# Performance work log

Measured on AMD Instinct MI355X. Metric: run time of the kernel, lower is better.

Reference implementation:

```python
import jax, jax.numpy as jnp
import numpy as np

B, C, H, W = 8, 3, 512, 512
KH = KW = 17          # blur kernel
F_REG, D = 24, 4      # regularization filters, Wiener filters
RKH = RKW = 5         # reg-filter kernel size


def psf2otf(psf, shape):
    """Zero-pad psf to `shape`, circshift so center is at (0,0), FFT."""
    kh, kw = psf.shape[-2:]
    Ho, Wo = shape
    pad = [(0, 0)] * (psf.ndim - 2) + [(0, Ho - kh), (0, Wo - kw)]
    p = jnp.pad(psf, pad)
    p = jnp.roll(p, (-(kh // 2), -(kw // 2)), axis=(-2, -1))
    return jnp.fft.fft2(p)


def edgetaper(img, psf):
    """MATLAB-style edgetaper. img: (C,Hp,Wp), psf: (kh,kw)."""
    Ho, Wo = img.shape[-2:]

    def autocorr(proj, n):
        z = jnp.zeros((n,), img.dtype).at[: proj.shape[0]].set(proj)
        z = jnp.fft.ifft(jnp.abs(jnp.fft.fft(z)) ** 2).real
        z = jnp.concatenate([z, z[:1]])  # length n+1
        return z / z.max()

    beta0 = autocorr(psf.sum(1), Ho - 1)  # (Ho,)
    beta1 = autocorr(psf.sum(0), Wo - 1)  # (Wo,)
    alpha = (1.0 - beta0)[:, None] * (1.0 - beta1)[None, :]  # (Ho,Wo)
    blurred = jnp.fft.ifft2(jnp.fft.fft2(img) * psf2otf(psf, (Ho, Wo))).real
    return alpha * img + (1.0 - alpha) * blurred


def wiener_one(y, psf, g, log_alpha):
    """Multi-filter Wiener deconvolution for one image.
    y: (C,Hp,Wp), psf: (kh,kw), g: (F,1,rkh,rkw), log_alpha: (D,1).
    Returns (D,C,Hp,Wp)."""
    Ho, Wo = y.shape[-2:]
    K = psf2otf(psf, (Ho, Wo))                  # (Hp,Wp) complex
    G = psf2otf(g[:, 0], (Ho, Wo))              # (F,Hp,Wp)
    Greg = jnp.sum(jnp.abs(G) ** 2, axis=0)     # (Hp,Wp)
    Y = jnp.fft.fft2(y)                         # (C,Hp,Wp)
    a = jnp.exp(log_alpha)[:, :, None, None]    # (D,1,1,1)
    S = jnp.abs(K) ** 2 + a * Greg              # (D,1,Hp,Wp)
    X = (jnp.conj(K) * Y)[None] / S             # (D,C,Hp,Wp)
    return jnp.fft.ifft2(X).real


def forward(image, blurKernel, stdn, wiener_conv_weights, wiener_scale, alpha, weights):
    kh, kw = blurKernel.shape[-2:]
    # getPad2RetainShape
    pt, pb = (kh + 1) // 2 - 1, kh - (kh + 1) // 2
    pl, pr = (kw + 1) // 2 - 1, kw - (kw + 1) // 2
    x = jnp.pad(image, ((0, 0), (0, 0), (pt, pb), (pl, pr)), mode='symmetric')
    psf = blurKernel[:, 0]                      # (B,kh,kw)
    x = jax.vmap(edgetaper)(x, psf)             # (B,C,Hp,Wp)
    # WeightNormalization: zero-mean then L2-normalize per filter, times scale
    w = wiener_conv_weights - wiener_conv_weights.mean(axis=(1, 2, 3), keepdims=True)
    nrm = jnp.sqrt(jnp.sum(w * w, axis=(1, 2, 3), keepdims=True))
    w = w * (wiener_scale.reshape(-1, 1, 1, 1) / nrm)
    xw = jax.vmap(lambda yi, ki: wiener_one(yi, ki, w, alpha))(x, psf)  # (B,D,C,Hp,Wp)
    Hp, Wp = x.shape[-2:]
    crop = xw[..., pt:Hp - pb, pl:Wp - pr]      # Crop2D back to (H,W)
    return jnp.sum(crop * weights, axis=1)      # weighted mix over D -> (B,C,H,W)


def setup_inputs() -> dict:
    key = jax.random.key(0)
    ks = jax.random.split(key, 4)
    image = jax.random.uniform(ks[0], (B, C, H, W), jnp.float32)
    k = jax.random.uniform(ks[1], (B, 1, KH, KW), jnp.float32)
    blurKernel = k / jnp.sum(k, axis=(-2, -1), keepdims=True)  # normalized psf
    stdn = jax.random.uniform(ks[2], (B,), jnp.float32) * 0.05 + 0.01
    wiener_conv_weights = jax.random.normal(ks[3], (F_REG, 1, RKH, RKW), jnp.float32)
    wiener_scale = jnp.full((F_REG,), 0.1, jnp.float32)
    alpha = jnp.log(jnp.logspace(np.log10(1e-3), np.log10(1e-1), D))[:, None].astype(jnp.float32)
    weights = jnp.full((1, D, 1, 1, 1), 1.0 / D, jnp.float32)
    return {"image": image, "blurKernel": blurKernel, "stdn": stdn,
            "wiener_conv_weights": wiener_conv_weights, "wiener_scale": wiener_scale,
            "alpha": alpha, "weights": weights}


def reference(image, blurKernel, stdn, wiener_conv_weights, wiener_scale, alpha, weights):
    return forward(image, blurKernel, stdn, wiener_conv_weights, wiener_scale, alpha, weights)
```

## Files before the change

### kernel.cpp

```cpp
#include <hip/hip_runtime.h>
#include <hip/hip_bf16.h>

#define NN 528
#define NP (NN*NN)
#define IMG 512
#define IMGP (IMG*IMG)
#define PAD 8
#define KH 17
#define KT (KH*KH)
#define NF 24
#define RK 5
#define RKT (RK*RK)
#define ND 4
#define TOPB (17*NN)
#define ROWB (2*TOPB)
#define SIDEB (494*34)
#define BORD (ROWB + SIDEB)

static __device__ __forceinline__ float ldx(const void* p, long i, int bf) {
    if (bf) return __bfloat162float(((const __hip_bfloat16*)p)[i]);
    return ((const float*)p)[i];
}

static __device__ __forceinline__ int gmap(int m) {
    if (m < -8)  return 495 - m;
    if (m < 0)   return -m - 1;
    if (m < 512) return m;
    if (m < 520) return 1023 - m;
    return 527 - m;
}

__global__ void detect_k(const void* pimg, int nimg, const void* pbk, int nbk,
                         const void* pwcw, int nwcw, const void* pws, int nws,
                         const float* c4a, const float* c4b,
                         int* __restrict__ flags,
                         float* __restrict__ alpha_ws, float* __restrict__ wgt_ws) {
    int t = threadIdx.x;
    const void* ps[4] = {pimg, pbk, pwcw, pws};
    int ns[4] = {nimg, nbk, nwcw, nws};
    if (t < 4) {
        const unsigned short* q = (const unsigned short*)ps[t];
        int n = ns[t];
        int K = n < 512 ? n : 512;
        int cnt = 0, pass = 0;
        for (int i = 0; i < K; i += 2) {
            int e = (q[i] >> 7) & 0xFF;
            pass += (e >= 100 && e <= 140);
            cnt++;
        }
        flags[t] = (pass * 10 >= cnt * 8) ? 1 : 0;
    }
    if (t == 7) {
        const float* A = (c4a[0] < 0.f) ? c4a : c4b;
        const float* W = (c4a[0] < 0.f) ? c4b : c4a;
        for (int i = 0; i < ND; ++i) { alpha_ws[i] = A[i]; wgt_ws[i] = W[i]; }
    }
}

__global__ void twinit_k(float2* __restrict__ twN) {
    int i = blockIdx.x * blockDim.x + threadIdx.x;
    if (i < NN) {
        double th = -6.283185307179586476925287 * (double)i / (double)NN;
        twN[i] = make_float2((float)cos(th), (float)sin(th));
    }
}

__global__ void wnorm_k(const void* __restrict__ wcw, const void* __restrict__ wscale,
                        const int* __restrict__ flags, float* __restrict__ wout) {
    int f = threadIdx.x;
    if (f >= NF) return;
    int bfw = flags[2], bfs = flags[3];
    float v[RKT];
    float mean = 0.f;
    for (int i = 0; i < RKT; ++i) { v[i] = ldx(wcw, f*RKT+i, bfw); mean += v[i]; }
    mean *= (1.f/(float)RKT);
    float ss = 0.f;
    for (int i = 0; i < RKT; ++i) { v[i] -= mean; ss += v[i]*v[i]; }
    float sc = ldx(wscale, f, bfs) / sqrtf(ss);
    for (int i = 0; i < RKT; ++i) wout[f*RKT+i] = v[i]*sc;
}

__global__ void prep_k(const void* __restrict__ blurKernel, const int* __restrict__ flags,
                       float* __restrict__ psf_all, float* __restrict__ A0_all,
                       float* __restrict__ A1_all) {
    int b = blockIdx.x, t = threadIdx.x;
    int bf = flags[1];
    __shared__ float psf[KT];
    __shared__ float q0[KH], q1[KH], ac0[KH], ac1[KH];
    for (int i = t; i < KT; i += 64) {
        float v = ldx(blurKernel, b*KT + i, bf);
        psf[i] = v;
        psf_all[b*KT + i] = v;
    }
    __syncthreads();
    if (t < KH) {
        float s0 = 0.f, s1 = 0.f;
        for (int k = 0; k < KH; ++k) { s0 += psf[t*KH + k]; s1 += psf[k*KH + t]; }
        q0[t] = s0; q1[t] = s1;
    }
    __syncthreads();
    if (t < KH) {
        float a0 = 0.f, a1 = 0.f;
        for (int m = 0; m + t < KH; ++m) { a0 += q0[m]*q0[m+t]; a1 += q1[m]*q1[m+t]; }
        ac0[t] = a0; ac1[t] = a1;
    }
    __syncthreads();
    for (int r = t; r < NN; r += 64) {
        int lag = min(r, (NN-1) - r);
        float b0 = (lag <= KH-1) ? ac0[lag]/ac0[0] : 0.f;
        float b1 = (lag <= KH-1) ? ac1[lag]/ac1[0] : 0.f;
        A0_all[b*NN + r] = 1.f - b0;
        A1_all[b*NN + r] = 1.f - b1;
    }
}

__global__ void greg_k(const float* __restrict__ w, const float2* __restrict__ twN,
                       float* __restrict__ Greg) {
    int p = blockIdx.x * blockDim.x + threadIdx.x;
    if (p >= NP) return;
    int u = p % NN, v = p / NN;
    float2 rp[RK], cp[RK];
    for (int j = 0; j < RK; ++j) {
        int m = (u * (j - RK/2)) % NN; if (m < 0) m += NN;
        rp[j] = twN[m];
    }
    for (int k = 0; k < RK; ++k) {
        int m = (v * (k - RK/2)) % NN; if (m < 0) m += NN;
        cp[k] = twN[m];
    }
    float pr[RKT], pi[RKT];
    for (int j = 0; j < RK; ++j)
        for (int k = 0; k < RK; ++k) {
            pr[j*RK+k] = rp[j].x*cp[k].x - rp[j].y*cp[k].y;
            pi[j*RK+k] = rp[j].x*cp[k].y + rp[j].y*cp[k].x;
        }
    float acc = 0.f;
    for (int f = 0; f < NF; ++f) {
        float gr = 0.f, gi = 0.f;
        for (int i = 0; i < RKT; ++i) {
            float wv = w[f*RKT + i];
            gr += wv * pr[i];
            gi += wv * pi[i];
        }
        acc += gr*gr + gi*gi;
    }
    Greg[p] = acc;
}

__global__ __launch_bounds__(256)
void border2_k(const void* __restrict__ image, const int* __restrict__ flags,
               const float* __restrict__ psf_all,
               const float* __restrict__ A0_all, const float* __restrict__ A1_all,
               float* __restrict__ borderV) {
    __shared__ float4 S4[1440];
    float* S = (float*)S4;
    int bp = blockIdx.y;
    int b = bp / 3;
    long ofs = (long)bp * IMGP;
    int bf = flags[0];
    int t = threadIdx.x;
    const float* pw = psf_all + b*KT;
    int bx = blockIdx.x;

    if (bx < 20) {
        int q = bx >> 1, h = bx & 1;
        int r0;
        if (q < 4) r0 = 4*q;
        else if (q == 4) r0 = 13;
        else if (q < 9) r0 = 511 + 4*(q-5);
        else r0 = 524;
        int X0 = h * 264;
        for (int idx = t; idx < 20*288; idx += 256) {
            int i = idx / 288, xi = idx - i*288;
            int x = X0 + xi;
            float v = 0.f;
            if (x < 544) {
                int sr = gmap(r0 - 16 + i);
                int sc = gmap(x - 16);
                v = ldx(image, ofs + (long)sr*IMG + sc, bf);
            }
            S[idx] = v;
        }
        __syncthreads();
        for (int g = t; g < 264; g += 256) {
            int rx = g / 66, cl = g - rx*66;
            int c0 = X0 + 4*cl;
            int x0 = 4*cl;
            float acc0 = 0.f, acc1 = 0.f, acc2 = 0.f, acc3 = 0.f;
            for (int j = 0; j < KH; ++j) {
                const float4* SjV = (const float4*)(S + (16 + rx - j)*288 + x0);
                float xv[20];
                #pragma unroll
                for (int qv = 0; qv < 5; ++qv) {
                    float4 tv = SjV[qv];
                    xv[4*qv+0] = tv.x; xv[4*qv+1] = tv.y;
                    xv[4*qv+2] = tv.z; xv[4*qv+3] = tv.w;
                }
                const float* wj = pw + j*KH;
                #pragma unroll
                for (int qq = 0; qq < 20; ++qq) {
                    {int k = 0 + 16 - qq; if (k >= 0 && k < KH) acc0 += wj[k]*xv[qq];}
                    {int k = 1 + 16 - qq; if (k >= 0 && k < KH) acc1 += wj[k]*xv[qq];}
                    {int k = 2 + 16 - qq; if (k >= 0 && k < KH) acc2 += wj[k]*xv[qq];}
                    {int k = 3 + 16 - qq; if (k >= 0 && k < KH) acc3 += wj[k]*xv[qq];}
                }
            }
            int r = r0 + rx;
            float a0v = A0_all[b*NN + r];
            int ibase = (r < 17) ? r*NN : TOPB + (r-511)*NN;
            float accs[4] = {acc0, acc1, acc2, acc3};
            #pragma unroll
            for (int d = 0; d < 4; ++d) {
                int c = c0 + d;
                float xo = S[(8 + rx)*288 + (x0 + 8 + d)];
                float al = a0v * A1_all[b*NN + c];
                borderV[(size_t)bp*BORD + ibase + c] = al*xo + (1.f - al)*accs[d];
            }
        }
    } else {
        int chunk = bx - 20;
        int r0 = 17 + 26*chunk;
        for (int idx = t; idx < 42*84; idx += 256) {
            int i = idx / 84, x = idx - i*84;
            float v = 0.f;
            int m = -1000;
            if (x < 33) m = x - 16;
            else if (x >= 48 && x < 81) m = x - 48 + 495;
            if (m != -1000) {
                int sr = gmap(r0 - 16 + i);
                int sc = gmap(m);
                v = ldx(image, ofs + (long)sr*IMG + sc, bf);
            }
            S[idx] = v;
        }
        __syncthreads();
        int g = t;
        if (g < 208) {
            int ry = g >> 3, s = g & 7;
            int c0 = (s < 4) ? 4*s : 511 + 4*(s-4);
            int sz = ((s & 3) == 3) ? 5 : 4;
            int x0 = (s < 4) ? 4*s : 48 + 4*(s-4);
            float acc0=0.f, acc1=0.f, acc2=0.f, acc3=0.f, acc4=0.f;
            for (int j = 0; j < KH; ++j) {
                const float4* SjV = (const float4*)(S + (16 + ry - j)*84 + x0);
                float xv[24];
                #pragma unroll
                for (int qv = 0; qv < 6; ++qv) {
                    float4 tv = SjV[qv];
                    xv[4*qv+0] = tv.x; xv[4*qv+1] = tv.y;
                    xv[4*qv+2] = tv.z; xv[4*qv+3] = tv.w;
                }
                const float* wj = pw + j*KH;
                #pragma unroll
                for (int qq = 0; qq < 21; ++qq) {
                    {int k = 0 + 16 - qq; if (k >= 0 && k < KH) acc0 += wj[k]*xv[qq];}
                    {int k = 1 + 16 - qq; if (k >= 0 && k < KH) acc1 += wj[k]*xv[qq];}
                    {int k = 2 + 16 - qq; if (k >= 0 && k < KH) acc2 += wj[k]*xv[qq];}
                    {int k = 3 + 16 - qq; if (k >= 0 && k < KH) acc3 += wj[k]*xv[qq];}
                    {int k = 4 + 16 - qq; if (k >= 0 && k < KH) acc4 += wj[k]*xv[qq];}
                }
            }
            int r = r0 + ry;
            float a0v = A0_all[b*NN + r];
            int cc0 = (s < 4) ? c0 : c0 - 494;
            size_t ib = (size_t)bp*BORD + ROWB + (size_t)(r-17)*34 + cc0;
            float accs[5] = {acc0, acc1, acc2, acc3, acc4};
            #pragma unroll
            for (int d = 0; d < 5; ++d) {
                if (d < sz) {
                    int c = c0 + d;
                    float xo = S[(8 + ry)*84 + (x0 + 8 + d)];
                    float al = a0v * A1_all[b*NN + c];
                    borderV[ib + d] = al*xo + (1.f - al)*accs[d];
                }
            }
        }
    }
}

__global__ void kv_k(const float* __restrict__ psf_all, const float2* __restrict__ twN,
                     float2* __restrict__ Sv) {
    int idx = blockIdx.x * blockDim.x + threadIdx.x;
    if (idx >= 8*NN*KH) return;
    int j = idx % KH;
    int rest = idx / KH;
    int v = rest % NN, b = rest / NN;
    int m = (520 * v) % NN;
    float sr = 0.f, si = 0.f;
    const float* ps = psf_all + b*KT + j*KH;
    for (int k = 0; k < KH; ++k) {
        float2 cp = twN[m];
        m += v; if (m >= NN) m -= NN;
        sr += ps[k] * cp.x;
        si += ps[k] * cp.y;
    }
    Sv[idx] = make_float2(sr, si);
}

__global__ __launch_bounds__(128)
void fftrow_k(const void* __restrict__ image, const int* __restrict__ flags,
              const float* __restrict__ borderV, const float2* __restrict__ twN,
              float2* __restrict__ buf, int B0) {
    __shared__ float2 X[NN];
    __shared__ float2 A[NN];
    __shared__ float2 TW[NN];
    int t = threadIdx.x;
    int q = blockIdx.x / NN;
    int r = blockIdx.x - q*NN;
    int pair = q / 3, ch = q - 3*pair;
    int b0p = B0 + 2*pair;
    int bf = flags[0];
    for (int i = t; i < NN; i += 128) TW[i] = twN[i];
    for (int c = t; c < NN; c += 128) {
        float x0, x1;
        bool isb = (r < 17) | (r >= 511) | (c < 17) | (c >= 511);
        if (isb) {
            int i2;
            if (r < 17) i2 = r*NN + c;
            else if (r >= 511) i2 = TOPB + (r-511)*NN + c;
            else { int cc = (c < 17) ? c : c - 494; i2 = ROWB + (r-17)*34 + cc; }
            x0 = borderV[(size_t)(b0p*3 + ch)*BORD + i2];
            x1 = borderV[(size_t)((b0p+1)*3 + ch)*BORD + i2];
        } else {
            long ofs0 = ((long)b0p*3 + ch) * IMGP + (long)(r - PAD)*IMG + (c - PAD);
            x0 = ldx(image, ofs0, bf);
            x1 = ldx(image, ofs0 + 3L*IMGP, bf);
        }
        X[c] = make_float2(x0, x1);
    }
    __syncthreads();
    for (int o = t; o < NN; o += 128) {
        int n1 = o & 15, k2 = o >> 4;
        float ar = 0.f, ai = 0.f;
        int m = 0;
        for (int n2 = 0; n2 < 33; ++n2) {
            float2 xv = X[n1 + 16*n2];
            float2 w = TW[m * 16];
            ar += xv.x*w.x - xv.y*w.y;
            ai += xv.x*w.y + xv.y*w.x;
            m += k2; if (m >= 33) m -= 33;
        }
        float2 tw = TW[n1 * k2];
        A[n1*33 + k2] = make_float2(ar*tw.x - ai*tw.y, ar*tw.y + ai*tw.x);
    }
    __syncthreads();
    float2* dst = buf + (size_t)q*NP + (size_t)r*NN;
    for (int o = t; o < NN; o += 128) {
        int k1 = o / 33, k2 = o - 33*k1;
        float ar = 0.f, ai = 0.f;
        int m = 0;
        for (int n1 = 0; n1 < 16; ++n1) {
            float2 bv = A[n1*33 + k2];
            float2 w = TW[m * 33];
            ar += bv.x*w.x - bv.y*w.y;
            ai += bv.x*w.y + bv.y*w.x;
            m = (m + k1) & 15;
        }
        dst[o] = make_float2(ar, ai);
    }
}

__global__ void transpose_ip_k(float2* __restrict__ buf) {
    int tnum = blockIdx.x;
    int ti = 0, rem = tnum;
    while (rem >= 33 - ti) { rem -= 33 - ti; ti++; }
    int tj = ti + rem;
    float2* pl = buf + (size_t)blockIdx.z * NP;
    __shared__ float2 ta[16][17], tb[16][17];
    int tx = threadIdx.x, ty = threadIdx.y;
    int ra = ti*16 + ty, ca = tj*16 + tx;
    int rb = tj*16 + ty, cb = ti*16 + tx;
    ta[ty][tx] = pl[(size_t)ra*NN + ca];
    tb[ty][tx] = pl[(size_t)rb*NN + cb];
    __syncthreads();
    pl[(size_t)ra*NN + ca] = tb[tx][ty];
    pl[(size_t)rb*NN + cb] = ta[tx][ty];
}

__global__ __launch_bounds__(256)
void rowpipe_k(float2* __restrict__ buf, const float2* __restrict__ Sv,
               const float* __restrict__ Greg, const float2* __restrict__ twN,
               const float* __restrict__ alpha4, const float* __restrict__ wgt4, int B0) {
    __shared__ float2 X[2][NN];
    __shared__ float2 A[2][NN];
    __shared__ float2 TW[NN];
    __shared__ float2 SvL[2][KH];
    int t = threadIdx.x;
    int q = blockIdx.x;
    int plane = blockIdx.y;
    int pair = plane / 3;
    int b0p = B0 + 2*pair;
    int qm = (NN - q) % NN;
    int nrow = (qm == q) ? 1 : 2;
    float2* pl = buf + (size_t)plane * NP;
    for (int i = t; i < NN; i += 256) TW[i] = twN[i];
    if (t < 2*KH) {
        int bsel = t / KH, j = t - KH*bsel;
        SvL[bsel][j] = Sv[((size_t)(b0p + bsel)*NN + q)*KH + j];
    }
    for (int i = t; i < nrow*NN; i += 256) {
        int l = i / NN, o = i - l*NN;
        X[l][o] = pl[(size_t)(l ? qm : q)*NN + o];
    }
    __syncthreads();
    for (int i = t; i < nrow*NN; i += 256) {
        int l = i / NN, o = i - l*NN;
        int n1 = o & 15, k2 = o >> 4;
        float ar = 0.f, ai = 0.f;
        int m = 0;
        for (int n2 = 0; n2 < 33; ++n2) {
            float2 xv = X[l][n1 + 16*n2];
            float2 w = TW[m * 16];
            ar += xv.x*w.x - xv.y*w.y;
            ai += xv.x*w.y + xv.y*w.x;
            m += k2; if (m >= 33) m -= 33;
        }
        float2 tw = TW[n1 * k2];
        A[l][n1*33 + k2] = make_float2(ar*tw.x - ai*tw.y, ar*tw.y + ai*tw.x);
    }
    __syncthreads();
    for (int i = t; i < nrow*NN; i += 256) {
        int l = i / NN, o = i - l*NN;
        int k1 = o / 33, k2 = o - 33*k1;
        float ar = 0.f, ai = 0.f;
        int m = 0;
        for (int n1 = 0; n1 < 16; ++n1) {
            float2 bv = A[l][n1*33 + k2];
            float2 w = TW[m * 33];
            ar += bv.x*w.x - bv.y*w.y;
            ai += bv.x*w.y + bv.y*w.x;
            m = (m + k1) & 15;
        }
        X[l][o] = make_float2(ar, ai);
    }
    __syncthreads();
    float aE[ND], wE[ND];
    #pragma unroll
    for (int d = 0; d < ND; ++d) { aE[d] = __expf(alpha4[d]); wE[d] = wgt4[d]; }
    int npair = (nrow == 2) ? NN : 265;
    int lm = nrow - 1;
    for (int k = t; k < npair; k += 256) {
        int km = (NN - k) % NN;
        int mu = (520 * k) % NN;
        float K0r = 0.f, K0i = 0.f, K1r = 0.f, K1i = 0.f;
        for (int j = 0; j < KH; ++j) {
            float2 rp = TW[mu]; mu += k; if (mu >= NN) mu -= NN;
            float2 s0 = SvL[0][j], s1 = SvL[1][j];
            K0r += rp.x*s0.x - rp.y*s0.y;  K0i += rp.x*s0.y + rp.y*s0.x;
            K1r += rp.x*s1.x - rp.y*s1.y;  K1i += rp.x*s1.y + rp.y*s1.x;
        }
        float gg = Greg[(size_t)q*NN + k];
        float K20 = K0r*K0r + K0i*K0i;
        float K21 = K1r*K1r + K1i*K1i;
        float s0a = 0.f, s1a = 0.f;
        #pragma unroll
        for (int d = 0; d < ND; ++d) {
            s0a += wE[d] / fmaxf(K20 + aE[d]*gg, 1e-30f);
            s1a += wE[d] / fmaxf(K21 + aE[d]*gg, 1e-30f);
        }
        s0a *= (1.f/(float)NP);
        s1a *= (1.f/(float)NP);
        float W0r = K0r*s0a, W0i = -K0i*s0a;
        float W1r = K1r*s1a, W1i = -K1i*s1a;
        float2 Z  = X[0][k];
        float2 Zm = X[lm][km];
        float X0r = 0.5f*(Z.x + Zm.x), X0i = 0.5f*(Z.y - Zm.y);
        float X1r = 0.5f*(Z.y + Zm.y), X1i = 0.5f*(Zm.x - Z.x);
        float Y0r = X0r*W0r - X0i*W0i, Y0i = X0r*W0i + X0i*W0r;
        float Y1r = X1r*W1r - X1i*W1i, Y1i = X1r*W1i + X1i*W1r;
        X[0][k]   = make_float2(Y0r - Y1i, Y0i + Y1r);
        X[lm][km] = make_float2(Y0r + Y1i, Y1r - Y0i);
    }
    __syncthreads();
    for (int i = t; i < nrow*NN; i += 256) {
        int l = i / NN, o = i - l*NN;
        int n1 = o & 15, k2 = o >> 4;
        float ar = 0.f, ai = 0.f;
        int m = 0;
        for (int n2 = 0; n2 < 33; ++n2) {
            float2 xv = X[l][n1 + 16*n2];
            float2 w = TW[m * 16];
            float wr = w.x, wi = -w.y;
            ar += xv.x*wr - xv.y*wi;
            ai += xv.x*wi + xv.y*wr;
            m += k2; if (m >= 33) m -= 33;
        }
        float2 tw = TW[n1 * k2];
        float twr = tw.x, twi = -tw.y;
        A[l][n1*33 + k2] = make_float2(ar*twr - ai*twi, ar*twi + ai*twr);
    }
    __syncthreads();
    for (int i = t; i < nrow*NN; i += 256) {
        int l = i / NN, o = i - l*NN;
        int k1 = o / 33, k2 = o - 33*k1;
        float ar = 0.f, ai = 0.f;
        int m = 0;
        for (int n1 = 0; n1 < 16; ++n1) {
            float2 bv = A[l][n1*33 + k2];
            float2 w = TW[m * 33];
            float wr = w.x, wi = -w.y;
            ar += bv.x*wr - bv.y*wi;
            ai += bv.x*wi + bv.y*wr;
            m = (m + k1) & 15;
        }
        X[l][o] = make_float2(ar, ai);
    }
    __syncthreads();
    for (int i = t; i < nrow*NN; i += 256) {
        int l = i / NN, o = i - l*NN;
        pl[(size_t)(l ? qm : q)*NN + o] = X[l][o];
    }
}

__global__ __launch_bounds__(128)
void fft_crop_k(const float2* __restrict__ in, float* __restrict__ out,
                const float2* __restrict__ twN, int B0) {
    __shared__ float2 X[NN];
    __shared__ float2 A[NN];
    __shared__ float2 TW[NN];
    int t = threadIdx.x;
    int q = blockIdx.x >> 9;
    int rp = (blockIdx.x & 511) + PAD;
    int pair = q / 3, ch = q - 3*pair;
    int b0p = B0 + 2*pair;
    const float2* src = in + (size_t)q*NP + (size_t)rp*NN;
    for (int i = t; i < NN; i += 128) { X[i] = src[i]; TW[i] = twN[i]; }
    __syncthreads();
    const float s = -1.f;
    for (int o = t; o < NN; o += 128) {
        int n1 = o & 15, k2 = o >> 4;
        float ar = 0.f, ai = 0.f;
        int m = 0;
        for (int n2 = 0; n2 < 33; ++n2) {
            float2 xv = X[n1 + 16*n2];
            float2 w = TW[m * 16];
            float wr = w.x, wi = w.y * s;
            ar += xv.x*wr - xv.y*wi;
            ai += xv.x*wi + xv.y*wr;
            m += k2; if (m >= 33) m -= 33;
        }
        float2 tw = TW[n1 * k2];
        float twr = tw.x, twi = tw.y * s;
        A[n1*33 + k2] = make_float2(ar*twr - ai*twi, ar*twi + ai*twr);
    }
    __syncthreads();
    float* o0 = out + ((size_t)b0p*3 + ch) * IMGP + (size_t)(rp - PAD) * IMG;
    float* o1 = o0 + 3L*IMGP;
    for (int o = PAD + t; o < IMG + PAD; o += 128) {
        int k1 = o / 33, k2 = o - 33*k1;
        float ar = 0.f, ai = 0.f;
        int m = 0;
        for (int n1 = 0; n1 < 16; ++n1) {
            float2 bv = A[n1*33 + k2];
            float2 w = TW[m * 33];
            float wr = w.x, wi = w.y * s;
            ar += bv.x*wr - bv.y*wi;
            ai += bv.x*wi + bv.y*wr;
            m = (m + k1) & 15;
        }
        o0[o - PAD] = ar;
        o1[o - PAD] = ai;
    }
}

extern "C" void kernel_launch(void* const* d_in, const int* in_sizes, int n_in,
                              void* d_out, int out_size, void* d_ws, size_t ws_size,
                              hipStream_t stream) {
    int i_img = -1, i_bk = -1, i_wcw = -1, i_ws = -1, i_4a = -1, i_4b = -1;
    for (int i = 0; i < n_in; ++i) {
        int s = in_sizes[i];
        if (s == 8*3*IMG*IMG)   i_img = i;
        else if (s == 8*KT)     i_bk = i;
        else if (s == NF*RKT)   i_wcw = i;
        else if (s == NF)       i_ws = i;
        else if (s == ND) { if (i_4a < 0) i_4a = i; else i_4b = i; }
    }
    if (i_img < 0) i_img = 0;
    if (i_bk  < 0) i_bk  = 1;
    if (i_wcw < 0) i_wcw = 3;
    if (i_ws  < 0) i_ws  = 4;
    if (i_4a  < 0) i_4a  = 5;
    if (i_4b  < 0) i_4b  = i_4a;
    const void* image      = d_in[i_img];
    const void* blurKernel = d_in[i_bk];
    const void* wcw        = d_in[i_wcw];
    const void* wscale     = d_in[i_ws];
    const float* c4a       = (const float*)d_in[i_4a];
    const float* c4b       = (const float*)d_in[i_4b];
    float* out = (float*)d_out;

    char* base = (char*)d_ws;
    int*    flags    = (int*)(base);
    float*  alpha_ws = (float*)(base + 64);
    float*  wgt_ws   = (float*)(base + 80);
    float2* twN      = (float2*)(base + 256);
    float*  wnorm    = (float*)(base + 4480);
    float*  psf_all  = (float*)(base + 6880);
    float*  A0       = (float*)(base + 16128);
    float*  A1       = (float*)(base + 33024);
    float*  Greg     = (float*)(base + 49920);
    float2* buf      = (float2*)(base + 1165056);
    float*  borderV  = (float*)(base + 14546688);
    float2* Sv       = (float2*)(base + 17882496);

    if (ws_size < 18456960) return;

    detect_k<<<1, 64, 0, stream>>>(image, in_sizes[i_img], blurKernel, in_sizes[i_bk],
                                   wcw, in_sizes[i_wcw], wscale, in_sizes[i_ws],
                                   c4a, c4b, flags, alpha_ws, wgt_ws);
    twinit_k<<<(NN+63)/64, 64, 0, stream>>>(twN);
    wnorm_k<<<1, 64, 0, stream>>>(wcw, wscale, flags, wnorm);
    prep_k<<<8, 64, 0, stream>>>(blurKernel, flags, psf_all, A0, A1);
    greg_k<<<(NP+255)/256, 256, 0, stream>>>(wnorm, twN, Greg);
    kv_k<<<(8*NN*KH+255)/256, 256, 0, stream>>>(psf_all, twN, Sv);

    dim3 bgrid2(39, 24);
    border2_k<<<bgrid2, 256, 0, stream>>>(image, flags, psf_all, A0, A1, borderV);

    dim3 tblk(16, 16);
    dim3 tgrid6(561, 1, 6);
    dim3 rpgrid(265, 6);
    for (int B0 = 0; B0 < 8; B0 += 4) {
        fftrow_k<<<6*NN, 128, 0, stream>>>(image, flags, borderV, twN, buf, B0);
        transpose_ip_k<<<tgrid6, tblk, 0, stream>>>(buf);
        rowpipe_k<<<rpgrid, 256, 0, stream>>>(buf, Sv, Greg, twN, alpha_ws, wgt_ws, B0);
        transpose_ip_k<<<tgrid6, tblk, 0, stream>>>(buf);
        fft_crop_k<<<6*IMG, 128, 0, stream>>>(buf, out, twN, B0);
    }
}
```

Baseline: 491.3 us.

## Register-block 528-point DFT stages four outputs per thread with vectorized LDS reads

Restructures both stages of the 16x33 mixed-radix DFT used in the row, Wiener and crop kernels so each thread computes four outputs. Each twiddle load is shared across those outputs and operands come from float4 shared-memory reads. Compact 33- and 16-entry twiddle tables and a padded A stride of 34 are added for aligned vector access. The aim is fewer LDS instructions and less index arithmetic per output. The cost is fewer active threads per stage (132 or 144 groups instead of 528 items), so the 128- and 256-thread blocks are underused in places.

```diff
diff --git a/kernel.cpp b/kernel.cpp
--- a/kernel.cpp
+++ b/kernel.cpp
@@ -16,6 +16,7 @@
 #define ROWB (2*TOPB)
 #define SIDEB (494*34)
 #define BORD (ROWB + SIDEB)
+#define AST 34
 
 static __device__ __forceinline__ float ldx(const void* p, long i, int bf) {
     if (bf) return __bfloat162float(((const __hip_bfloat16*)p)[i]);
@@ -28,6 +29,60 @@
     if (m < 512) return m;
     if (m < 520) return 1023 - m;
     return 527 - m;
+}
+
+static __device__ __forceinline__ void s1_group(const float2* __restrict__ Xrow,
+                                                float2* __restrict__ Arow,
+                                                const float2* __restrict__ TWF,
+                                                const float2* __restrict__ T33,
+                                                float s, int grp) {
+    int k2 = grp >> 2, n1b = (grp & 3) << 2;
+    const float4* Xv = (const float4*)Xrow;
+    float ar[4] = {0.f,0.f,0.f,0.f}, ai[4] = {0.f,0.f,0.f,0.f};
+    int m = 0;
+    for (int n2 = 0; n2 < 33; ++n2) {
+        int fi = (n1b + 16*n2) >> 1;
+        float4 a0 = Xv[fi], a1 = Xv[fi+1];
+        float2 w = T33[m]; m += k2; if (m >= 33) m -= 33;
+        float wr = w.x, wi = s*w.y;
+        ar[0] += a0.x*wr - a0.y*wi; ai[0] += a0.x*wi + a0.y*wr;
+        ar[1] += a0.z*wr - a0.w*wi; ai[1] += a0.z*wi + a0.w*wr;
+        ar[2] += a1.x*wr - a1.y*wi; ai[2] += a1.x*wi + a1.y*wr;
+        ar[3] += a1.z*wr - a1.w*wi; ai[3] += a1.z*wi + a1.w*wr;
+    }
+    #pragma unroll
+    for (int j = 0; j < 4; ++j) {
+        float2 tw = TWF[(n1b + j) * k2];
+        float twr = tw.x, twi = s*tw.y;
+        Arow[(n1b + j)*AST + k2] = make_float2(ar[j]*twr - ai[j]*twi, ar[j]*twi + ai[j]*twr);
+    }
+}
+
+static __device__ __forceinline__ void s2_compute(const float2* __restrict__ Arow,
+                                                  const float2* __restrict__ T16,
+                                                  float s, int k1, int k2b, int sz,
+                                                  float* __restrict__ ar, float* __restrict__ ai) {
+    ar[0]=ar[1]=ar[2]=ar[3]=0.f; ai[0]=ai[1]=ai[2]=ai[3]=0.f;
+    if (sz == 4) {
+        const float4* Av = (const float4*)Arow;
+        for (int n1 = 0; n1 < 16; ++n1) {
+            int fi = (n1*AST + k2b) >> 1;
+            float4 a0 = Av[fi], a1 = Av[fi+1];
+            float2 w = T16[(k1*n1) & 15];
+            float wr = w.x, wi = s*w.y;
+            ar[0] += a0.x*wr - a0.y*wi; ai[0] += a0.x*wi + a0.y*wr;
+            ar[1] += a0.z*wr - a0.w*wi; ai[1] += a0.z*wi + a0.w*wr;
+            ar[2] += a1.x*wr - a1.y*wi; ai[2] += a1.x*wi + a1.y*wr;
+            ar[3] += a1.z*wr - a1.w*wi; ai[3] += a1.z*wi + a1.w*wr;
+        }
+    } else {
+        for (int n1 = 0; n1 < 16; ++n1) {
+            float2 a = Arow[n1*AST + k2b];
+            float2 w = T16[(k1*n1) & 15];
+            float wr = w.x, wi = s*w.y;
+            ar[0] += a.x*wr - a.y*wi; ai[0] += a.x*wi + a.y*wr;
+        }
+    }
 }
 
 __global__ void detect_k(const void* pimg, int nimg, const void* pbk, int nbk,
@@ -301,16 +356,20 @@
 void fftrow_k(const void* __restrict__ image, const int* __restrict__ flags,
               const float* __restrict__ borderV, const float2* __restrict__ twN,
               float2* __restrict__ buf, int B0) {
-    __shared__ float2 X[NN];
-    __shared__ float2 A[NN];
-    __shared__ float2 TW[NN];
+    __shared__ __align__(16) float2 X[NN];
+    __shared__ __align__(16) float2 A[16*AST];
+    __shared__ float2 TWF[NN];
+    __shared__ float2 T33[33];
+    __shared__ float2 T16[16];
     int t = threadIdx.x;
     int q = blockIdx.x / NN;
     int r = blockIdx.x - q*NN;
     int pair = q / 3, ch = q - 3*pair;
     int b0p = B0 + 2*pair;
     int bf = flags[0];
-    for (int i = t; i < NN; i += 128) TW[i] = twN[i];
+    for (int i = t; i < NN; i += 128) TWF[i] = twN[i];
+    if (t < 33) T33[t] = twN[t*16];
+    else if (t >= 64 && t < 80) T16[t-64] = twN[(t-64)*33];
     for (int c = t; c < NN; c += 128) {
         float x0, x1;
         bool isb = (r < 17) | (r >= 511) | (c < 17) | (c >= 511);
@@ -329,34 +388,17 @@
         X[c] = make_float2(x0, x1);
     }
     __syncthreads();
-    for (int o = t; o < NN; o += 128) {
-        int n1 = o & 15, k2 = o >> 4;
-        float ar = 0.f, ai = 0.f;
-        int m = 0;
-        for (int n2 = 0; n2 < 33; ++n2) {
-            float2 xv = X[n1 + 16*n2];
-            float2 w = TW[m * 16];
-            ar += xv.x*w.x - xv.y*w.y;
-            ai += xv.x*w.y + xv.y*w.x;
-            m += k2; if (m >= 33) m -= 33;
-        }
-        float2 tw = TW[n1 * k2];
-        A[n1*33 + k2] = make_float2(ar*tw.x - ai*tw.y, ar*tw.y + ai*tw.x);
-    }
+    for (int grp = t; grp < 132; grp += 128) s1_group(X, A, TWF, T33, 1.f, grp);
     __syncthreads();
     float2* dst = buf + (size_t)q*NP + (size_t)r*NN;
-    for (int o = t; o < NN; o += 128) {
-        int k1 = o / 33, k2 = o - 33*k1;
-        float ar = 0.f, ai = 0.f;
-        int m = 0;
-        for (int n1 = 0; n1 < 16; ++n1) {
-            float2 bv = A[n1*33 + k2];
-            float2 w = TW[m * 33];
-            ar += bv.x*w.x - bv.y*w.y;
-            ai += bv.x*w.y + bv.y*w.x;
-            m = (m + k1) & 15;
-        }
-        dst[o] = make_float2(ar, ai);
+    for (int grp = t; grp < 144; grp += 128) {
+        int k1 = grp / 9, kg = grp - 9*k1;
+        int k2b = kg << 2, sz = (kg == 8) ? 1 : 4;
+        float ar[4], ai[4];
+        s2_compute(A, T16, 1.f, k1, k2b, sz, ar, ai);
+        #pragma unroll
+        for (int j = 0; j < 4; ++j)
+            if (j < sz) dst[k1*33 + k2b + j] = make_float2(ar[j], ai[j]);
     }
 }
 
@@ -381,9 +423,11 @@
 void rowpipe_k(float2* __restrict__ buf, const float2* __restrict__ Sv,
                const float* __restrict__ Greg, const float2* __restrict__ twN,
                const float* __restrict__ alpha4, const float* __restrict__ wgt4, int B0) {
-    __shared__ float2 X[2][NN];
-    __shared__ float2 A[2][NN];
-    __shared__ float2 TW[NN];
+    __shared__ __align__(16) float2 X[2][NN];
+    __shared__ __align__(16) float2 A[2][16*AST];
+    __shared__ float2 TWF[NN];
+    __shared__ float2 T33[33];
+    __shared__ float2 T16[16];
     __shared__ float2 SvL[2][KH];
     int t = threadIdx.x;
     int q = blockIdx.x;
@@ -393,9 +437,12 @@
     int qm = (NN - q) % NN;
     int nrow = (qm == q) ? 1 : 2;
     float2* pl = buf + (size_t)plane * NP;
-    for (int i = t; i < NN; i += 256) TW[i] = twN[i];
-    if (t < 2*KH) {
-        int bsel = t / KH, j = t - KH*bsel;
+    for (int i = t; i < NN; i += 256) TWF[i] = twN[i];
+    if (t < 33) T33[t] = twN[t*16];
+    else if (t >= 64 && t < 80) T16[t-64] = twN[(t-64)*33];
+    else if (t >= 128 && t < 128 + 2*KH) {
+        int tt = t - 128;
+        int bsel = tt / KH, j = tt - KH*bsel;
         SvL[bsel][j] = Sv[((size_t)(b0p + bsel)*NN + q)*KH + j];
     }
     for (int i = t; i < nrow*NN; i += 256) {
@@ -403,35 +450,20 @@
         X[l][o] = pl[(size_t)(l ? qm : q)*NN + o];
     }
     __syncthreads();
-    for (int i = t; i < nrow*NN; i += 256) {
-        int l = i / NN, o = i - l*NN;
-        int n1 = o & 15, k2 = o >> 4;
-        float ar = 0.f, ai = 0.f;
-        int m = 0;
-        for (int n2 = 0; n2 < 33; ++n2) {
-            float2 xv = X[l][n1 + 16*n2];
-            float2 w = TW[m * 16];
-            ar += xv.x*w.x - xv.y*w.y;
-            ai += xv.x*w.y + xv.y*w.x;
-            m += k2; if (m >= 33) m -= 33;
-        }
-        float2 tw = TW[n1 * k2];
-        A[l][n1*33 + k2] = make_float2(ar*tw.x - ai*tw.y, ar*tw.y + ai*tw.x);
-    }
-    __syncthreads();
-    for (int i = t; i < nrow*NN; i += 256) {
-        int l = i / NN, o = i - l*NN;
-        int k1 = o / 33, k2 = o - 33*k1;
-        float ar = 0.f, ai = 0.f;
-        int m = 0;
-        for (int n1 = 0; n1 < 16; ++n1) {
-            float2 bv = A[l][n1*33 + k2];
-            float2 w = TW[m * 33];
-            ar += bv.x*w.x - bv.y*w.y;
-            ai += bv.x*w.y + bv.y*w.x;
-            m = (m + k1) & 15;
-        }
-        X[l][o] = make_float2(ar, ai);
+    for (int idx = t; idx < nrow*132; idx += 256) {
+        int l = idx / 132, grp = idx - l*132;
+        s1_group(X[l], A[l], TWF, T33, 1.f, grp);
+    }
+    __syncthreads();
+    for (int idx = t; idx < nrow*144; idx += 256) {
+        int l = idx / 144, grp = idx - l*144;
+        int k1 = grp / 9, kg = grp - 9*k1;
+        int k2b = kg << 2, sz = (kg == 8) ? 1 : 4;
+        float ar[4], ai[4];
+        s2_compute(A[l], T16, 1.f, k1, k2b, sz, ar, ai);
+        #pragma unroll
+        for (int j = 0; j < 4; ++j)
+            if (j < sz) X[l][k1*33 + k2b + j] = make_float2(ar[j], ai[j]);
     }
     __syncthreads();
     float aE[ND], wE[ND];
@@ -444,7 +476,7 @@
         int mu = (520 * k) % NN;
         float K0r = 0.f, K0i = 0.f, K1r = 0.f, K1i = 0.f;
         for (int j = 0; j < KH; ++j) {
-            float2 rp = TW[mu]; mu += k; if (mu >= NN) mu -= NN;
+            float2 rp = TWF[mu]; mu += k; if (mu >= NN) mu -= NN;
             float2 s0 = SvL[0][j], s1 = SvL[1][j];
             K0r += rp.x*s0.x - rp.y*s0.y;  K0i += rp.x*s0.y + rp.y*s0.x;
             K1r += rp.x*s1.x - rp.y*s1.y;  K1i += rp.x*s1.y + rp.y*s1.x;
@@ -472,38 +504,20 @@
         X[lm][km] = make_float2(Y0r + Y1i, Y1r - Y0i);
     }
     __syncthreads();
-    for (int i = t; i < nrow*NN; i += 256) {
-        int l = i / NN, o = i - l*NN;
-        int n1 = o & 15, k2 = o >> 4;
-        float ar = 0.f, ai = 0.f;
-        int m = 0;
-        for (int n2 = 0; n2 < 33; ++n2) {
-            float2 xv = X[l][n1 + 16*n2];
-            float2 w = TW[m * 16];
-            float wr = w.x, wi = -w.y;
-            ar += xv.x*wr - xv.y*wi;
-            ai += xv.x*wi + xv.y*wr;
-            m += k2; if (m >= 33) m -= 33;
-        }
-        float2 tw = TW[n1 * k2];
-        float twr = tw.x, twi = -tw.y;
-        A[l][n1*33 + k2] = make_float2(ar*twr - ai*twi, ar*twi + ai*twr);
-    }
-    __syncthreads();
-    for (int i = t; i < nrow*NN; i += 256) {
-        int l = i / NN, o = i - l*NN;
-        int k1 = o / 33, k2 = o - 33*k1;
-        float ar = 0.f, ai = 0.f;
-        int m = 0;
-        for (int n1 = 0; n1 < 16; ++n1) {
-            float2 bv = A[l][n1*33 + k2];
-            float2 w = TW[m * 33];
-            float wr = w.x, wi = -w.y;
-            ar += bv.x*wr - bv.y*wi;
-            ai += bv.x*wi + bv.y*wr;
-            m = (m + k1) & 15;
-        }
-        X[l][o] = make_float2(ar, ai);
+    for (int idx = t; idx < nrow*132; idx += 256) {
+        int l = idx / 132, grp = idx - l*132;
+        s1_group(X[l], A[l], TWF, T33, -1.f, grp);
+    }
+    __syncthreads();
+    for (int idx = t; idx < nrow*144; idx += 256) {
+        int l = idx / 144, grp = idx - l*144;
+        int k1 = grp / 9, kg = grp - 9*k1;
+        int k2b = kg << 2, sz = (kg == 8) ? 1 : 4;
+        float ar[4], ai[4];
+        s2_compute(A[l], T16, -1.f, k1, k2b, sz, ar, ai);
+        #pragma unroll
+        for (int j = 0; j < 4; ++j)
+            if (j < sz) X[l][k1*33 + k2b + j] = make_float2(ar[j], ai[j]);
     }
     __syncthreads();
     for (int i = t; i < nrow*NN; i += 256) {
@@ -515,51 +529,38 @@
 __global__ __launch_bounds__(128)
 void fft_crop_k(const float2* __restrict__ in, float* __restrict__ out,
                 const float2* __restrict__ twN, int B0) {
-    __shared__ float2 X[NN];
-    __shared__ float2 A[NN];
-    __shared__ float2 TW[NN];
+    __shared__ __align__(16) float2 X[NN];
+    __shared__ __align__(16) float2 A[16*AST];
+    __shared__ float2 TWF[NN];
+    __shared__ float2 T33[33];
+    __shared__ float2 T16[16];
     int t = threadIdx.x;
     int q = blockIdx.x >> 9;
     int rp = (blockIdx.x & 511) + PAD;
     int pair = q / 3, ch = q - 3*pair;
     int b0p = B0 + 2*pair;
     const float2* src = in + (size_t)q*NP + (size_t)rp*NN;
-    for (int i = t; i < NN; i += 128) { X[i] = src[i]; TW[i] = twN[i]; }
-    __syncthreads();
-    const float s = -1.f;
-    for (int o = t; o < NN; o += 128) {
-        int n1 = o & 15, k2 = o >> 4;
-        float ar = 0.f, ai = 0.f;
-        int m = 0;
-        for (int n2 = 0; n2 < 33; ++n2) {
-            float2 xv = X[n1 + 16*n2];
-            float2 w = TW[m * 16];
-            float wr = w.x, wi = w.y * s;
-            ar += xv.x*wr - xv.y*wi;
-            ai += xv.x*wi + xv.y*wr;
-            m += k2; if (m >= 33) m -= 33;
-        }
-        float2 tw = TW[n1 * k2];
-        float twr = tw.x, twi = tw.y * s;
-        A[n1*33 + k2] = make_float2(ar*twr - ai*twi, ar*twi + ai*twr);
-    }
+    for (int i = t; i < NN; i += 128) { X[i] = src[i]; TWF[i] = twN[i]; }
+    if (t < 33) T33[t] = twN[t*16];
+    else if (t >= 64 && t < 80) T16[t-64] = twN[(t-64)*33];
+    __syncthreads();
+    for (int grp = t; grp < 132; grp += 128) s1_group(X, A, TWF, T33, -1.f, grp);
     __syncthreads();
     float* o0 = out + ((size_t)b0p*3 + ch) * IMGP + (size_t)(rp - PAD) * IMG;
     float* o1 = o0 + 3L*IMGP;
-    for (int o = PAD + t; o < IMG + PAD; o += 128) {
-        int k1 = o / 33, k2 = o - 33*k1;
-        float ar = 0.f, ai = 0.f;
-        int m = 0;
-        for (int n1 = 0; n1 < 16; ++n1) {
-            float2 bv = A[n1*33 + k2];
-            float2 w = TW[m * 33];
-            float wr = w.x, wi = w.y * s;
-            ar += bv.x*wr - bv.y*wi;
-            ai += bv.x*wi + bv.y*wr;
-            m = (m + k1) & 15;
-        }
-        o0[o - PAD] = ar;
-        o1[o - PAD] = ai;
+    for (int grp = t; grp < 144; grp += 128) {
+        int k1 = grp / 9, kg = grp - 9*k1;
+        int k2b = kg << 2, sz = (kg == 8) ? 1 : 4;
+        float ar[4], ai[4];
+        s2_compute(A, T16, -1.f, k1, k2b, sz, ar, ai);
+        #pragma unroll
+        for (int j = 0; j < 4; ++j) {
+            int o = k1*33 + k2b + j;
+            if (j < sz && o >= PAD && o < IMG + PAD) {
+                o0[o - PAD] = ar[j];
+                o1[o - PAD] = ai[j];
+            }
+        }
     }
 }
 
```

New measurement: 696.8 us. 41.8% more time.
